# Kernel optimization log

Hardware: AMD Instinct MI355X
Metric: run time of the kernel (lower is better)

## Reference

```python
import jax, jax.numpy as jnp
import numpy as np

MASK_THR = 0.2
EPS = 1e-12  # torch F.normalize eps


def setup_inputs() -> dict:
    key = jax.random.key(0)
    k1, k2, k3 = jax.random.split(key, 3)
    B, Cin, H, W = 2, 384, 96, 96
    features = jax.random.normal(k1, (B, Cin, H, W), dtype=jnp.float32)
    # projector: Conv2d(384,256,1) -> ReLU -> Conv2d(256,128,1); 1x1 convs == per-pixel GEMMs
    W1 = jax.random.normal(k2, (256, Cin), dtype=jnp.float32) * (1.0 / np.sqrt(Cin))
    b1 = jnp.zeros((256,), dtype=jnp.float32)
    W2 = jax.random.normal(k3, (128, 256), dtype=jnp.float32) * (1.0 / np.sqrt(256))
    b2 = jnp.zeros((128,), dtype=jnp.float32)
    return {"features": features, "W1": W1, "b1": b1, "W2": W2, "b2": b2}


def reference(features, W1, b1, W2, b2):
    B, _, H, Wd = features.shape
    # projector (1x1 convs as channel GEMMs)
    h = jax.nn.relu(jnp.einsum('oc,bchw->bohw', W1, features) + b1[None, :, None, None])
    feat = jnp.einsum('oc,bchw->bohw', W2, h) + b2[None, :, None, None]  # [B,128,H,W]
    # get_mask: L2-normalize over channels, full pairwise similarity, top-2 NN, distance, threshold
    norm = jnp.sqrt(jnp.sum(feat * feat, axis=1, keepdims=True))
    nf = feat / jnp.maximum(norm, EPS)
    C = nf.shape[1]
    rf = jnp.transpose(nf, (0, 2, 3, 1)).reshape(B, H * Wd, C)         # [B,N,C]
    sim = jnp.einsum('bnc,bmc->bnm', rf, rf)                           # [B,N,N]
    _, top2_idx = jax.lax.top_k(sim, 2)
    nn_idx = top2_idx[:, :, 1]                                         # nearest non-self neighbor
    nearest = jnp.take_along_axis(rf, nn_idx[:, :, None], axis=1)      # [B,N,C]
    diff = rf - nearest
    distance = jnp.sqrt(jnp.sum(diff * diff, axis=-1))                 # [B,N]
    mask = (distance > MASK_THR).astype(feat.dtype).reshape(B, 1, H, Wd)
    return mask, distance
```

## Files before the change

kernel.cpp:

```cpp
#include <hip/hip_runtime.h>

#define NHW 9216
#define NB 2
#define NCHUNK 16

typedef short s8v __attribute__((ext_vector_type(8)));
typedef _Float16 h8v __attribute__((ext_vector_type(8)));
typedef float f4v __attribute__((ext_vector_type(4)));
typedef int i4v __attribute__((ext_vector_type(4)));
typedef unsigned int u32;
typedef unsigned short u16;

#define QSCALE 181.0f
#define IBIAS  2097152

__device__ inline u16 f2h(float x) {
    _Float16 h = (_Float16)x;
    return *(u16*)&h;
}

__device__ inline void wait_barrier() {
    asm volatile("s_waitcnt vmcnt(0)" ::: "memory");
    __builtin_amdgcn_s_barrier();
    __builtin_amdgcn_sched_barrier(0);
}

__global__ __launch_bounds__(256) void k_xsplit(const float* __restrict__ X,
                                                const float* __restrict__ W1,
                                                const float* __restrict__ W2,
                                                u16* __restrict__ xh,
                                                u16* __restrict__ w1h, u16* __restrict__ w1l,
                                                u16* __restrict__ w2h)
{
    __shared__ float fs[64][65];
    const int tid = threadIdx.x;
    const int b = blockIdx.z, p0 = blockIdx.x * 64, half = blockIdx.y;

    {
        int flat = ((b * 2 + half) * 144 + blockIdx.x) * 256 + tid;
        if (flat < 98304) {
            float v = W1[flat];
            _Float16 h = (_Float16)v;
            w1h[flat] = *(u16*)&h;
            w1l[flat] = f2h(v - (float)h);
        } else if (flat < 131072) {
            int j = flat - 98304;
            w2h[j] = f2h(W2[j]);
        }
    }

    const size_t fb = (size_t)b * 384 * NHW;
    const int px = tid >> 2, sub = tid & 3;
    const size_t g = (size_t)b * NHW + p0 + px;
    for (int pass = half * 3; pass < half * 3 + 3; ++pass) {
        int c0p = pass * 64;
        __syncthreads();
#pragma unroll
        for (int r = 0; r < 16; ++r) {
            int e = r * 256 + tid;
            int cc = e >> 6, p = e & 63;
            fs[cc][p] = X[fb + (size_t)(c0p + cc) * NHW + p0 + p];
        }
        __syncthreads();
        u16 hb[16];
#pragma unroll
        for (int i = 0; i < 16; ++i) hb[i] = f2h(fs[sub * 16 + i][px]);
        size_t o = g * 384 + c0p + sub * 16;
        *(s8v*)&xh[o]     = *(s8v*)&hb[0];
        *(s8v*)&xh[o + 8] = *(s8v*)&hb[8];
    }
}

__global__ __launch_bounds__(256, 4) void k_gemm1(const u16* __restrict__ xh,
                                                  const u16* __restrict__ w1h, const u16* __restrict__ w1l,
                                                  const float* __restrict__ b1,
                                                  u16* __restrict__ hh)
{
    union __align__(16) SM {
        struct { u16 B[2][16][512]; } stg;
        u16 bounce[128 * 66];
    };
    __shared__ SM sm;
    const int tid = threadIdx.x;
    const int wave = tid >> 6, l = tid & 63, l15 = l & 15, q = l >> 4;
    const int bx = blockIdx.x;
    const int xcd = bx & 7, k = bx >> 3;
    const int g0 = (xcd * 18 + (k >> 2)) * 128;
    const int c0 = (k & 3) * 64;
    const int gw = g0 + wave * 32;

    auto stage = [&](int kt, int buf) {
#pragma unroll
        for (int r = 0; r < 4; ++r) {
            int cid = r * 4 + wave;
            int spl = cid >> 3, kf = (cid >> 2) & 1, cs = cid & 3;
            const u16* src = (spl ? w1l : w1h) + (size_t)(c0 + cs * 16 + l15) * 384 + kt + kf * 32 + q * 8;
            __builtin_amdgcn_global_load_lds(
                (const __attribute__((address_space(1))) void*)src,
                (__attribute__((address_space(3))) void*)&sm.stg.B[buf][cid][0],
                16, 0, 0);
        }
    };

    f4v acc[2][4];
#pragma unroll
    for (int s = 0; s < 2; ++s)
#pragma unroll
        for (int c = 0; c < 4; ++c) acc[s][c] = (f4v){0.f, 0.f, 0.f, 0.f};

    stage(0, 0);
    for (int t = 0; t < 6; ++t) {
        const int kt = t * 64;
        const int buf = t & 1;
        wait_barrier();
        s8v ah[2][2];
#pragma unroll
        for (int s = 0; s < 2; ++s)
#pragma unroll
            for (int kf = 0; kf < 2; ++kf)
                ah[s][kf] = *(const s8v*)&xh[(size_t)(gw + s * 16 + l15) * 384 + kt + kf * 32 + q * 8];
        if (t < 5) stage(kt + 64, buf ^ 1);
#pragma unroll
        for (int kf = 0; kf < 2; ++kf)
#pragma unroll
            for (int cs = 0; cs < 4; ++cs) {
                s8v bh = *(const s8v*)&sm.stg.B[buf][kf * 4 + cs][l * 8];
                s8v bl = *(const s8v*)&sm.stg.B[buf][8 + kf * 4 + cs][l * 8];
#pragma unroll
                for (int s = 0; s < 2; ++s) {
                    acc[s][cs] = __builtin_amdgcn_mfma_f32_16x16x32_f16(*(h8v*)&ah[s][kf], *(h8v*)&bh, acc[s][cs], 0, 0, 0);
                    acc[s][cs] = __builtin_amdgcn_mfma_f32_16x16x32_f16(*(h8v*)&ah[s][kf], *(h8v*)&bl, acc[s][cs], 0, 0, 0);
                }
            }
    }
    __syncthreads();

#pragma unroll
    for (int s = 0; s < 2; ++s)
#pragma unroll
        for (int cs = 0; cs < 4; ++cs) {
            int c = cs * 16 + l15;
            float bv = b1[c0 + c];
#pragma unroll
            for (int r = 0; r < 4; ++r) {
                int px = wave * 32 + s * 16 + q * 4 + r;
                sm.bounce[px * 66 + c] = f2h(fmaxf(acc[s][cs][r] + bv, 0.f));
            }
        }
    __syncthreads();
    {
        int px = tid >> 1, half = tid & 1;
        u32 tmp[16];
#pragma unroll
        for (int j = 0; j < 16; ++j)
            tmp[j] = *(const u32*)&sm.bounce[px * 66 + half * 32 + j * 2];
        size_t o = (size_t)(g0 + px) * 256 + c0 + half * 32;
#pragma unroll
        for (int j = 0; j < 4; ++j)
            *(s8v*)&hh[o + j * 8] = ((s8v*)tmp)[j];
    }
}

__global__ __launch_bounds__(256) void k_gemm2n(const u16* __restrict__ hh,
                                                const u16* __restrict__ w2h,
                                                const float* __restrict__ b2,
                                                float* __restrict__ rf,
                                                signed char* __restrict__ qi8)
{
    __shared__ u16 Bs[64][512];
    const int tid = threadIdx.x;
    const int wave = tid >> 6, l = tid & 63, l15 = l & 15, q = l >> 4;
    const int bx = blockIdx.x;
    const int xcd = bx & 7, k = bx >> 3;
    const int g0 = (xcd * 36 + k) * 64;

#pragma unroll
    for (int r = 0; r < 16; ++r) {
        int cid = r * 4 + wave;
        int kf = cid >> 3, cst = cid & 7;
        const u16* src = w2h + (size_t)(cst * 16 + l15) * 256 + kf * 32 + q * 8;
        __builtin_amdgcn_global_load_lds(
            (const __attribute__((address_space(1))) void*)src,
            (__attribute__((address_space(3))) void*)&Bs[cid][0],
            16, 0, 0);
    }
    __syncthreads();

    const int gw = g0 + wave * 16;
    f4v acc[8];
#pragma unroll
    for (int c = 0; c < 8; ++c) acc[c] = (f4v){0.f, 0.f, 0.f, 0.f};

#pragma unroll
    for (int kf = 0; kf < 8; ++kf) {
        s8v ah = *(const s8v*)&hh[(size_t)(gw + l15) * 256 + kf * 32 + q * 8];
#pragma unroll
        for (int cst = 0; cst < 8; ++cst) {
            s8v bh = *(const s8v*)&Bs[kf * 8 + cst][l * 8];
            acc[cst] = __builtin_amdgcn_mfma_f32_16x16x32_f16(*(h8v*)&ah, *(h8v*)&bh, acc[cst], 0, 0, 0);
        }
    }

    float ssq[4] = {0.f, 0.f, 0.f, 0.f};
#pragma unroll
    for (int cst = 0; cst < 8; ++cst) {
        float bv = b2[cst * 16 + l15];
#pragma unroll
        for (int r = 0; r < 4; ++r) {
            acc[cst][r] += bv;
            ssq[r] += acc[cst][r] * acc[cst][r];
        }
    }
#pragma unroll
    for (int r = 0; r < 4; ++r) {
        ssq[r] += __shfl_xor(ssq[r], 1, 64);
        ssq[r] += __shfl_xor(ssq[r], 2, 64);
        ssq[r] += __shfl_xor(ssq[r], 4, 64);
        ssq[r] += __shfl_xor(ssq[r], 8, 64);
        ssq[r] = 1.0f / fmaxf(sqrtf(ssq[r]), 1e-12f);
    }
#pragma unroll
    for (int cst = 0; cst < 8; ++cst)
#pragma unroll
        for (int r = 0; r < 4; ++r) {
            float val = acc[cst][r] * ssq[r];
            size_t o = (size_t)(gw + q * 4 + r) * 128 + cst * 16 + l15;
            rf[o] = val;
            int qv = __float2int_rn(fminf(fmaxf(val * QSCALE, -127.f), 127.f));
            qi8[o] = (signed char)qv;
        }
}

__global__ __launch_bounds__(256, 4) void k_simtop(const signed char* __restrict__ qi,
                                                   int* __restrict__ cidx)
{
    __shared__ signed char Bs[2][8][1024];
    const int tid  = threadIdx.x;
    const int wave = tid >> 6, l = tid & 63, l15 = l & 15, q = l >> 4;
    const int b     = blockIdx.z;
    const int rbase = blockIdx.x * 128;
    const int chunk = blockIdx.y;
    const int cbase = chunk * 576;
    const size_t base = (size_t)b * NHW;
    const int wr0 = rbase + wave * 32;

    i4v ah[2][2];
#pragma unroll
    for (int s = 0; s < 2; ++s) {
        int row = wr0 + s * 16 + l15;
#pragma unroll
        for (int kf = 0; kf < 2; ++kf)
            ah[s][kf] = *(const i4v*)&qi[(base + row) * 128 + kf * 64 + q * 16];
    }

    auto stage = [&](int colt, int buf) {
#pragma unroll
        for (int r = 0; r < 2; ++r) {
            int cid = r * 4 + wave;
            int kf = cid >> 2, cs = cid & 3;
            int col = colt + cs * 16 + l15;
            const signed char* src = qi + (base + col) * 128 + kf * 64 + q * 16;
            __builtin_amdgcn_global_load_lds(
                (const __attribute__((address_space(1))) void*)src,
                (__attribute__((address_space(3))) void*)&Bs[buf][cid][0],
                16, 0, 0);
        }
    };

    u32 bk[2][4];
#pragma unroll
    for (int s = 0; s < 2; ++s)
#pragma unroll
        for (int r = 0; r < 4; ++r) bk[s][r] = 0u;

    stage(cbase, 0);

    for (int ct = 0; ct < 9; ++ct) {
        const int colt = cbase + ct * 64;
        const int buf  = ct & 1;
        wait_barrier();
        if (ct < 8) stage(colt + 64, buf ^ 1);

        i4v acc[2][4];
#pragma unroll
        for (int s = 0; s < 2; ++s)
#pragma unroll
            for (int c = 0; c < 4; ++c) acc[s][c] = (i4v){IBIAS, IBIAS, IBIAS, IBIAS};

#pragma unroll
        for (int kf = 0; kf < 2; ++kf)
#pragma unroll
            for (int cs = 0; cs < 4; ++cs) {
                i4v bh = *(const i4v*)&Bs[buf][kf * 4 + cs][l * 16];
#pragma unroll
                for (int s = 0; s < 2; ++s)
                    acc[s][cs] = __builtin_amdgcn_mfma_i32_16x16x64_i8(ah[s][kf], bh, acc[s][cs], 0, 0, 0);
            }

        const u32 tagv = (u32)(ct << 2);
        const bool hasdiag = (colt < wr0 + 32) && (wr0 < colt + 64);
        if (hasdiag) {
#pragma unroll
            for (int s = 0; s < 2; ++s)
#pragma unroll
                for (int r = 0; r < 4; ++r) {
                    const int rr = wr0 + s * 16 + q * 4 + r;
                    u32 km = 0u;
#pragma unroll
                    for (int cs = 0; cs < 4; ++cs) {
                        u32 kk = ((u32)acc[s][cs][r] << 6) | (tagv | (u32)cs);
                        if (colt + cs * 16 + l15 == rr) kk = 0u;
                        km = kk > km ? kk : km;
                    }
                    bk[s][r] = km > bk[s][r] ? km : bk[s][r];
                }
        } else {
#pragma unroll
            for (int s = 0; s < 2; ++s)
#pragma unroll
                for (int r = 0; r < 4; ++r) {
                    u32 km = 0u;
#pragma unroll
                    for (int cs = 0; cs < 4; ++cs) {
                        u32 kk = ((u32)acc[s][cs][r] << 6) | (tagv | (u32)cs);
                        km = kk > km ? kk : km;
                    }
                    bk[s][r] = km > bk[s][r] ? km : bk[s][r];
                }
        }
    }

#pragma unroll
    for (int s = 0; s < 2; ++s)
#pragma unroll
        for (int r = 0; r < 4; ++r) {
            u32 key = bk[s][r];
            int sv = (int)(key >> 6);
            int ctw = (int)((key >> 2) & 15u);
            int csw = (int)(key & 3u);
            int col = cbase + ctw * 64 + csw * 16 + l15;
#pragma unroll
            for (int d = 1; d < 16; d <<= 1) {
                int ov = __shfl_xor(sv, d, 64);
                int oi = __shfl_xor(col, d, 64);
                bool p = (ov > sv) || (ov == sv && oi < col);
                sv  = p ? ov : sv;
                col = p ? oi : col;
            }
            if (l15 == 0) {
                int row = wr0 + s * 16 + q * 4 + r;
                cidx[(base + row) * NCHUNK + chunk] = col;
            }
        }
}

__global__ __launch_bounds__(256) void k_finish(const float* __restrict__ rf,
                                                const int* __restrict__ cidx,
                                                float* __restrict__ out)
{
    const int tid = threadIdx.x;
    const int g = blockIdx.x * 16 + (tid >> 4);
    const int l15 = tid & 15;
    const int b = g / NHW;
    const size_t rowbase = (size_t)b * NHW;

    const float* x = rf + (size_t)g * 128;
    f4v x0 = *(const f4v*)&x[l15 * 8];
    f4v x1 = *(const f4v*)&x[l15 * 8 + 4];

    float bestS = -2.f; int bestI = 0;
#pragma unroll
    for (int j = 0; j < NCHUNK; ++j) {
        int c = cidx[(size_t)g * NCHUNK + j];
        const float* y = rf + (rowbase + c) * 128;
        f4v y0 = *(const f4v*)&y[l15 * 8];
        f4v y1 = *(const f4v*)&y[l15 * 8 + 4];
        float s = x0[0]*y0[0] + x0[1]*y0[1] + x0[2]*y0[2] + x0[3]*y0[3]
                + x1[0]*y1[0] + x1[1]*y1[1] + x1[2]*y1[2] + x1[3]*y1[3];
#pragma unroll
        for (int d = 1; d < 16; d <<= 1) s += __shfl_xor(s, d, 64);
        bool p = (s > bestS) || (s == bestS && c < bestI);
        bestS = p ? s : bestS;
        bestI = p ? c : bestI;
    }

    const float* y = rf + (rowbase + bestI) * 128;
    f4v y0 = *(const f4v*)&y[l15 * 8];
    f4v y1 = *(const f4v*)&y[l15 * 8 + 4];
    float d0 = x0[0]-y0[0], d1 = x0[1]-y0[1], d2 = x0[2]-y0[2], d3 = x0[3]-y0[3];
    float e0 = x1[0]-y1[0], e1 = x1[1]-y1[1], e2 = x1[2]-y1[2], e3 = x1[3]-y1[3];
    float ss = d0*d0 + d1*d1 + d2*d2 + d3*d3 + e0*e0 + e1*e1 + e2*e2 + e3*e3;
#pragma unroll
    for (int d = 1; d < 16; d <<= 1) ss += __shfl_xor(ss, d, 64);
    if (l15 == 0) {
        float dist = sqrtf(ss);
        out[NB * NHW + g] = dist;
        out[g] = dist > 0.2f ? 1.0f : 0.0f;
    }
}

extern "C" void kernel_launch(void* const* d_in, const int* in_sizes, int n_in,
                              void* d_out, int out_size, void* d_ws, size_t ws_size,
                              hipStream_t stream) {
    const float* features = (const float*)d_in[0];
    const float* W1 = (const float*)d_in[1];
    const float* b1 = (const float*)d_in[2];
    const float* W2 = (const float*)d_in[3];
    const float* b2 = (const float*)d_in[4];
    float* out = (float*)d_out;
    float* ws  = (float*)d_ws;

    u16*   xh   = (u16*)ws;
    u16*   hh   = (u16*)(ws + 3538944);
    u16*   w1h  = (u16*)(ws + 5898240);
    u16*   w1l  = (u16*)(ws + 5947392);
    u16*   w2h  = (u16*)(ws + 5996544);
    float* rf   = ws;
    signed char* qi8 = (signed char*)(ws + 2359296);
    int*   cidx = (int*)(ws + 3538944);

    k_xsplit<<<dim3(144, 2, NB), 256, 0, stream>>>(features, W1, W2, xh, w1h, w1l, w2h);
    k_gemm1<<<576, 256, 0, stream>>>(xh, w1h, w1l, b1, hh);
    k_gemm2n<<<288, 256, 0, stream>>>(hh, w2h, b2, rf, qi8);
    k_simtop<<<dim3(72, NCHUNK, NB), 256, 0, stream>>>(qi8, cidx);
    k_finish<<<1152, 256, 0, stream>>>(rf, cidx, out);
}
```

Baseline: 162.5 us.

## Fuse fp32-to-fp16 conversion of inputs and weights into GEMM kernels

```diff
diff --git a/kernel.cpp b/kernel.cpp
--- a/kernel.cpp
+++ b/kernel.cpp
@@ -19,65 +19,25 @@
     return *(u16*)&h;
 }
 
+__device__ inline void lds_barrier() {
+    asm volatile("s_waitcnt lgkmcnt(0)" ::: "memory");
+    __builtin_amdgcn_s_barrier();
+    __builtin_amdgcn_sched_barrier(0);
+}
+
 __device__ inline void wait_barrier() {
     asm volatile("s_waitcnt vmcnt(0)" ::: "memory");
     __builtin_amdgcn_s_barrier();
     __builtin_amdgcn_sched_barrier(0);
 }
 
-__global__ __launch_bounds__(256) void k_xsplit(const float* __restrict__ X,
-                                                const float* __restrict__ W1,
-                                                const float* __restrict__ W2,
-                                                u16* __restrict__ xh,
-                                                u16* __restrict__ w1h, u16* __restrict__ w1l,
-                                                u16* __restrict__ w2h)
-{
-    __shared__ float fs[64][65];
-    const int tid = threadIdx.x;
-    const int b = blockIdx.z, p0 = blockIdx.x * 64, half = blockIdx.y;
-
-    {
-        int flat = ((b * 2 + half) * 144 + blockIdx.x) * 256 + tid;
-        if (flat < 98304) {
-            float v = W1[flat];
-            _Float16 h = (_Float16)v;
-            w1h[flat] = *(u16*)&h;
-            w1l[flat] = f2h(v - (float)h);
-        } else if (flat < 131072) {
-            int j = flat - 98304;
-            w2h[j] = f2h(W2[j]);
-        }
-    }
-
-    const size_t fb = (size_t)b * 384 * NHW;
-    const int px = tid >> 2, sub = tid & 3;
-    const size_t g = (size_t)b * NHW + p0 + px;
-    for (int pass = half * 3; pass < half * 3 + 3; ++pass) {
-        int c0p = pass * 64;
-        __syncthreads();
-#pragma unroll
-        for (int r = 0; r < 16; ++r) {
-            int e = r * 256 + tid;
-            int cc = e >> 6, p = e & 63;
-            fs[cc][p] = X[fb + (size_t)(c0p + cc) * NHW + p0 + p];
-        }
-        __syncthreads();
-        u16 hb[16];
-#pragma unroll
-        for (int i = 0; i < 16; ++i) hb[i] = f2h(fs[sub * 16 + i][px]);
-        size_t o = g * 384 + c0p + sub * 16;
-        *(s8v*)&xh[o]     = *(s8v*)&hb[0];
-        *(s8v*)&xh[o + 8] = *(s8v*)&hb[8];
-    }
-}
-
-__global__ __launch_bounds__(256, 4) void k_gemm1(const u16* __restrict__ xh,
-                                                  const u16* __restrict__ w1h, const u16* __restrict__ w1l,
+__global__ __launch_bounds__(256, 2) void k_gemm1(const float* __restrict__ X,
+                                                  const float* __restrict__ W1,
                                                   const float* __restrict__ b1,
                                                   u16* __restrict__ hh)
 {
     union __align__(16) SM {
-        struct { u16 B[2][16][512]; } stg;
+        struct { u16 Xs[128][72]; u16 Ws[16][512]; } stg;
         u16 bounce[128 * 66];
     };
     __shared__ SM sm;
@@ -85,47 +45,83 @@
     const int wave = tid >> 6, l = tid & 63, l15 = l & 15, q = l >> 4;
     const int bx = blockIdx.x;
     const int xcd = bx & 7, k = bx >> 3;
-    const int g0 = (xcd * 18 + (k >> 2)) * 128;
+    const int pg = xcd * 18 + (k >> 2);
     const int c0 = (k & 3) * 64;
-    const int gw = g0 + wave * 32;
-
-    auto stage = [&](int kt, int buf) {
-#pragma unroll
-        for (int r = 0; r < 4; ++r) {
-            int cid = r * 4 + wave;
-            int spl = cid >> 3, kf = (cid >> 2) & 1, cs = cid & 3;
-            const u16* src = (spl ? w1l : w1h) + (size_t)(c0 + cs * 16 + l15) * 384 + kt + kf * 32 + q * 8;
-            __builtin_amdgcn_global_load_lds(
-                (const __attribute__((address_space(1))) void*)src,
-                (__attribute__((address_space(3))) void*)&sm.stg.B[buf][cid][0],
-                16, 0, 0);
+    const int bb = pg >= 72 ? 1 : 0;
+    const int hw0 = (pg - bb * 72) * 128;
+    const int g0 = pg * 128;
+    const size_t xbase = (size_t)bb * 384 * NHW + hw0;
+
+    const int xk8 = tid & 7;
+    const int xpx = (tid >> 3) * 4;
+
+    f4v xl[8];
+    f4v wl[2][2];
+
+    auto do_load = [&](int kt) {
+#pragma unroll
+        for (int kr = 0; kr < 8; ++kr)
+            xl[kr] = *(const f4v*)&X[xbase + (size_t)(kt + xk8 * 8 + kr) * NHW + xpx];
+#pragma unroll
+        for (int i = 0; i < 2; ++i) {
+            int p = tid * 2 + i;
+            int co = p & 63, ko = p >> 6;
+            const float* src = &W1[(size_t)(c0 + co) * 384 + kt + ko * 8];
+            wl[i][0] = *(const f4v*)&src[0];
+            wl[i][1] = *(const f4v*)&src[4];
         }
     };
 
+    auto do_write = [&]() {
+#pragma unroll
+        for (int j = 0; j < 4; ++j) {
+            u16 hv[8];
+#pragma unroll
+            for (int kr = 0; kr < 8; ++kr) hv[kr] = f2h(xl[kr][j]);
+            *(s8v*)&sm.stg.Xs[xpx + j][xk8 * 8] = *(s8v*)hv;
+        }
+#pragma unroll
+        for (int i = 0; i < 2; ++i) {
+            int p = tid * 2 + i;
+            int co = p & 63, ko = p >> 6;
+            int cs = co >> 4, lc = co & 15, kf = ko >> 2, qk = ko & 3;
+            u16 hi[8], lo[8];
+#pragma unroll
+            for (int e = 0; e < 8; ++e) {
+                float v = wl[i][e >> 2][e & 3];
+                _Float16 h = (_Float16)v;
+                hi[e] = *(u16*)&h;
+                lo[e] = f2h(v - (float)h);
+            }
+            *(s8v*)&sm.stg.Ws[kf * 4 + cs][(qk * 16 + lc) * 8] = *(s8v*)hi;
+            *(s8v*)&sm.stg.Ws[8 + kf * 4 + cs][(qk * 16 + lc) * 8] = *(s8v*)lo;
+        }
+    };
+
     f4v acc[2][4];
 #pragma unroll
     for (int s = 0; s < 2; ++s)
 #pragma unroll
         for (int c = 0; c < 4; ++c) acc[s][c] = (f4v){0.f, 0.f, 0.f, 0.f};
 
-    stage(0, 0);
+    do_load(0);
     for (int t = 0; t < 6; ++t) {
-        const int kt = t * 64;
-        const int buf = t & 1;
-        wait_barrier();
+        lds_barrier();
+        do_write();
+        lds_barrier();
+        if (t < 5) do_load((t + 1) * 64);
         s8v ah[2][2];
 #pragma unroll
         for (int s = 0; s < 2; ++s)
 #pragma unroll
             for (int kf = 0; kf < 2; ++kf)
-                ah[s][kf] = *(const s8v*)&xh[(size_t)(gw + s * 16 + l15) * 384 + kt + kf * 32 + q * 8];
-        if (t < 5) stage(kt + 64, buf ^ 1);
+                ah[s][kf] = *(const s8v*)&sm.stg.Xs[wave * 32 + s * 16 + l15][kf * 32 + q * 8];
 #pragma unroll
         for (int kf = 0; kf < 2; ++kf)
 #pragma unroll
             for (int cs = 0; cs < 4; ++cs) {
-                s8v bh = *(const s8v*)&sm.stg.B[buf][kf * 4 + cs][l * 8];
-                s8v bl = *(const s8v*)&sm.stg.B[buf][8 + kf * 4 + cs][l * 8];
+                s8v bh = *(const s8v*)&sm.stg.Ws[kf * 4 + cs][l * 8];
+                s8v bl = *(const s8v*)&sm.stg.Ws[8 + kf * 4 + cs][l * 8];
 #pragma unroll
                 for (int s = 0; s < 2; ++s) {
                     acc[s][cs] = __builtin_amdgcn_mfma_f32_16x16x32_f16(*(h8v*)&ah[s][kf], *(h8v*)&bh, acc[s][cs], 0, 0, 0);
@@ -162,7 +158,7 @@
 }
 
 __global__ __launch_bounds__(256) void k_gemm2n(const u16* __restrict__ hh,
-                                                const u16* __restrict__ w2h,
+                                                const float* __restrict__ W2,
                                                 const float* __restrict__ b2,
                                                 float* __restrict__ rf,
                                                 signed char* __restrict__ qi8)
@@ -175,14 +171,17 @@
     const int g0 = (xcd * 36 + k) * 64;
 
 #pragma unroll
-    for (int r = 0; r < 16; ++r) {
-        int cid = r * 4 + wave;
-        int kf = cid >> 3, cst = cid & 7;
-        const u16* src = w2h + (size_t)(cst * 16 + l15) * 256 + kf * 32 + q * 8;
-        __builtin_amdgcn_global_load_lds(
-            (const __attribute__((address_space(1))) void*)src,
-            (__attribute__((address_space(3))) void*)&Bs[cid][0],
-            16, 0, 0);
+    for (int i = 0; i < 16; ++i) {
+        int p = i * 256 + tid;
+        int c = p & 127, k8g = p >> 7;
+        const float* src = &W2[(size_t)c * 256 + k8g * 8];
+        f4v a0 = *(const f4v*)&src[0];
+        f4v a1 = *(const f4v*)&src[4];
+        u16 hv[8];
+#pragma unroll
+        for (int e = 0; e < 4; ++e) { hv[e] = f2h(a0[e]); hv[4 + e] = f2h(a1[e]); }
+        int cst = c >> 4, lc = c & 15, kf = k8g >> 2, qk = k8g & 3;
+        *(s8v*)&Bs[kf * 8 + cst][(qk * 16 + lc) * 8] = *(s8v*)hv;
     }
     __syncthreads();
 
@@ -410,18 +409,13 @@
     float* out = (float*)d_out;
     float* ws  = (float*)d_ws;
 
-    u16*   xh   = (u16*)ws;
-    u16*   hh   = (u16*)(ws + 3538944);
-    u16*   w1h  = (u16*)(ws + 5898240);
-    u16*   w1l  = (u16*)(ws + 5947392);
-    u16*   w2h  = (u16*)(ws + 5996544);
     float* rf   = ws;
     signed char* qi8 = (signed char*)(ws + 2359296);
-    int*   cidx = (int*)(ws + 3538944);
-
-    k_xsplit<<<dim3(144, 2, NB), 256, 0, stream>>>(features, W1, W2, xh, w1h, w1l, w2h);
-    k_gemm1<<<576, 256, 0, stream>>>(xh, w1h, w1l, b1, hh);
-    k_gemm2n<<<288, 256, 0, stream>>>(hh, w2h, b2, rf, qi8);
+    u16*   hh   = (u16*)(ws + 2949120);
+    int*   cidx = (int*)(ws + 5308416);
+
+    k_gemm1<<<576, 256, 0, stream>>>(features, W1, b1, hh);
+    k_gemm2n<<<288, 256, 0, stream>>>(hh, W2, b2, rf, qi8);
     k_simtop<<<dim3(72, NCHUNK, NB), 256, 0, stream>>>(qi8, cidx);
     k_finish<<<1152, 256, 0, stream>>>(rf, cidx, out);
 }
```

New measurement: 164.5 us. About the same (+1.3%).
